# Optimization experiments

Hardware: AMD Instinct MI355X
Metric: run time of the kernel (lower is better)

## Reference

```python
import jax, jax.numpy as jnp
import numpy as np

N_NODES = 100000
DEG = 16
D_IN = 128
D_OUT = 128


def setup_inputs() -> dict:
    key = jax.random.key(0)
    k1, k2, k3, k4, k5, k6 = jax.random.split(key, 6)
    neighbours = jax.random.randint(k1, (N_NODES, DEG), 0, N_NODES, dtype=jnp.int64 if jax.config.jax_enable_x64 else jnp.int32)
    shape_features = jax.random.normal(k2, (N_NODES, D_IN), dtype=jnp.float32)
    scale = 1.0 / np.sqrt(D_IN)
    W1 = jax.random.normal(k3, (D_OUT, D_IN), dtype=jnp.float32) * scale
    b1 = jax.random.normal(k4, (D_OUT,), dtype=jnp.float32) * scale
    W2 = jax.random.normal(k5, (D_OUT, D_IN), dtype=jnp.float32) * scale
    b2 = jax.random.normal(k6, (D_OUT,), dtype=jnp.float32) * scale
    return {"neighbours": neighbours, "shape_features": shape_features,
            "W1": W1, "b1": b1, "W2": W2, "b2": b2}


def reference(neighbours, shape_features, W1, b1, W2, b2):
    # linear1(x): x @ W1^T + b1  -> [N, D_OUT]
    out1 = jnp.einsum('nd,od->no', shape_features, W1) + b1
    # per-node neighbor gather + sum (vectorized form of the Python loop)
    # gathered: [N, DEG, D_IN], aggr: [N, D_IN]
    aggr = shape_features[neighbours].sum(axis=1)
    out = out1 + jnp.einsum('nd,od->no', aggr, W2) + b2
    return jax.nn.relu(out)
```

## Files before the change

kernel.cpp:

```cpp
#include <hip/hip_runtime.h>
#include <hip/hip_bf16.h>
#include <stdint.h>


#define N_NODES 100000
#define DEG 16
#define KTOT 256
#define M_PAD 100096

typedef __attribute__((ext_vector_type(8))) short short8;
typedef __attribute__((ext_vector_type(4))) float floatx4;

static __device__ __forceinline__ unsigned short f2bf(float f) {
  union { float f; uint32_t u; } v; v.f = f;
  uint32_t u = v.u;
  return (unsigned short)((u + 0x7fffu + ((u >> 16) & 1u)) >> 16);
}
static __device__ __forceinline__ float bf2f(uint32_t bits16) {
  union { uint32_t u; float f; } v; v.u = bits16 << 16; return v.f;
}

__global__ __launch_bounds__(256) void k_prep(const float* __restrict__ W1, const float* __restrict__ b1,
                                              const float* __restrict__ W2, const float* __restrict__ b2,
                                              unsigned short* __restrict__ Bt, float* __restrict__ bias) {
  int t = blockIdx.x * 256 + threadIdx.x;
  int o = t >> 8, k = t & 255;
  float v = (k < 128) ? W1[o * 128 + k] : W2[o * 128 + (k - 128)];
  Bt[t] = f2bf(v);
  if (t < 128) bias[t] = b1[t] + b2[t];
}

__global__ __launch_bounds__(256) void k_convert(const float* __restrict__ x,
                                                 unsigned short* __restrict__ A) {
  int t = blockIdx.x * 256 + threadIdx.x;
  if (t >= N_NODES * 32) return;
  int n = t >> 5, c4 = t & 31;
  float4 v = *(const float4*)(x + (size_t)n * 128 + (size_t)c4 * 4);
  ushort4 o;
  o.x = f2bf(v.x); o.y = f2bf(v.y); o.z = f2bf(v.z); o.w = f2bf(v.w);
  *(ushort4*)(A + (size_t)n * 256 + (size_t)c4 * 4) = o;
}

__global__ __launch_bounds__(256) void k_aggr(const int* __restrict__ nbrs,
                                              unsigned short* __restrict__ A) {
  int gid = blockIdx.x * 4 + (threadIdx.x >> 6);
  int lane = threadIdx.x & 63;
  int myidx = nbrs[(size_t)gid * DEG + (lane & 15)];
  float a0 = 0.f, a1 = 0.f;
#pragma unroll
  for (int j = 0; j < DEG; ++j) {
    int nb = __shfl(myidx, j);
    uint32_t pv = *(const uint32_t*)(A + (size_t)nb * 256 + (size_t)lane * 2);
    a0 += bf2f(pv & 0xffffu);
    a1 += bf2f(pv >> 16);
  }
  uint32_t w = (uint32_t)f2bf(a0) | ((uint32_t)f2bf(a1) << 16);
  *(uint32_t*)(A + (size_t)gid * 256 + 128 + (size_t)lane * 2) = w;
}

__global__ __launch_bounds__(256) void k_gemm(const unsigned short* __restrict__ A,
                                              const unsigned short* __restrict__ Bt,
                                              const float* __restrict__ bias,
                                              float* __restrict__ out) {
  __shared__ unsigned short lds[16384];
  const int tid = threadIdx.x;
  const int lane = tid & 63;
  const int w = tid >> 6;
  const int wm = w >> 1, wn = w & 1;
  const size_t tile_m = (size_t)blockIdx.x * 128;

  floatx4 acc[4][4];
#pragma unroll
  for (int i = 0; i < 4; ++i)
#pragma unroll
    for (int j = 0; j < 4; ++j) acc[i][j] = (floatx4){0.f, 0.f, 0.f, 0.f};

  const int l8 = lane >> 3;
  const int slot_sw = (lane & 7) ^ l8;
  const unsigned short* Ag = A + tile_m * 256;

  for (int kt = 0; kt < 4; ++kt) {
    __syncthreads();
#pragma unroll
    for (int p = 0; p < 4; ++p) {
      int row = p * 32 + w * 8 + l8;
      const unsigned short* g = Ag + (size_t)row * 256 + kt * 64 + slot_sw * 8;
      __builtin_amdgcn_global_load_lds((const __attribute__((address_space(1))) uint32_t*)g,
                                       (__attribute__((address_space(3))) uint32_t*)&lds[(p * 4 + w) * 512],
                                       16, 0, 0);
    }
#pragma unroll
    for (int p = 0; p < 4; ++p) {
      int row = p * 32 + w * 8 + l8;
      const unsigned short* g = Bt + (size_t)row * 256 + kt * 64 + slot_sw * 8;
      __builtin_amdgcn_global_load_lds((const __attribute__((address_space(1))) uint32_t*)g,
                                       (__attribute__((address_space(3))) uint32_t*)&lds[8192 + (p * 4 + w) * 512],
                                       16, 0, 0);
    }
    __syncthreads();

#pragma unroll
    for (int ks = 0; ks < 2; ++ks) {
      short8 a[4], b[4];
      const int kb = ks * 64 + (lane >> 4) * 16;
      const int swz = (lane & 7) << 4;
#pragma unroll
      for (int mi = 0; mi < 4; ++mi) {
        int row = wm * 64 + mi * 16 + (lane & 15);
        a[mi] = *(const short8*)((const char*)lds + row * 128 + (kb ^ swz));
      }
#pragma unroll
      for (int ni = 0; ni < 4; ++ni) {
        int row = wn * 64 + ni * 16 + (lane & 15);
        b[ni] = *(const short8*)((const char*)lds + 16384 + row * 128 + (kb ^ swz));
      }
#pragma unroll
      for (int mi = 0; mi < 4; ++mi)
#pragma unroll
        for (int ni = 0; ni < 4; ++ni)
          acc[mi][ni] = __builtin_amdgcn_mfma_f32_16x16x32_bf16(a[mi], b[ni], acc[mi][ni], 0, 0, 0);
    }
  }

  float bcol[4];
#pragma unroll
  for (int ni = 0; ni < 4; ++ni) bcol[ni] = bias[wn * 64 + ni * 16 + (lane & 15)];
  const int r0 = (lane >> 4) * 4;
#pragma unroll
  for (int mi = 0; mi < 4; ++mi) {
    size_t mbase = tile_m + wm * 64 + mi * 16 + r0;
#pragma unroll
    for (int r = 0; r < 4; ++r) {
      size_t mrow = mbase + r;
      if (mrow < N_NODES) {
        float* orow = out + mrow * 128 + wn * 64 + (lane & 15);
#pragma unroll
        for (int ni = 0; ni < 4; ++ni) {
          float vv = acc[mi][ni][r] + bcol[ni];
          orow[ni * 16] = vv > 0.f ? vv : 0.f;
        }
      }
    }
  }
}

extern "C" void kernel_launch(void* const* d_in, const int* in_sizes, int n_in,
                              void* d_out, int out_size, void* d_ws, size_t ws_size,
                              hipStream_t stream) {
  const int* nbrs  = (const int*)d_in[0];
  const float* x   = (const float*)d_in[1];
  const float* W1  = (const float*)d_in[2];
  const float* b1  = (const float*)d_in[3];
  const float* W2  = (const float*)d_in[4];
  const float* b2  = (const float*)d_in[5];
  float* out = (float*)d_out;

  unsigned short* A  = (unsigned short*)d_ws;
  unsigned short* Bt = A + (size_t)M_PAD * 256;
  float* bias = (float*)(Bt + 128 * 256);

  k_prep<<<128, 256, 0, stream>>>(W1, b1, W2, b2, Bt, bias);
  k_convert<<<12500, 256, 0, stream>>>(x, A);
  k_aggr<<<25000, 256, 0, stream>>>(nbrs, A);
  k_gemm<<<782, 256, 0, stream>>>(A, Bt, bias, out);
}
```

Baseline: 183.2 us.

## Fuse neighbour aggregation into GEMM tile and merge weight prep into convert

The neighbour gather-sum now runs inside the GEMM kernel. Each block aggregates its 128 nodes straight into LDS as bf16 and feeds them to MFMA as the second half of K, so the separate aggregation kernel and its global write and re-read of the aggregated half of A go away. The bf16 feature buffer shrinks to 128 columns, weight and bias prep is folded into the convert kernel as extra blocks, and B fragments are loaded straight from global memory instead of being staged through LDS. MFMA runs at raised wave priority, with occupancy set to 3 blocks per CU. The cost is that the GEMM can no longer start until each block has done its own latency-bound gathers, and it now uses 48KB of LDS per block.

```diff
diff --git a/kernel.cpp b/kernel.cpp
--- a/kernel.cpp
+++ b/kernel.cpp
@@ -1,11 +1,9 @@
 #include <hip/hip_runtime.h>
-#include <hip/hip_bf16.h>
 #include <stdint.h>
 
 
 #define N_NODES 100000
 #define DEG 16
-#define KTOT 256
 #define M_PAD 100096
 
 typedef __attribute__((ext_vector_type(8))) short short8;
@@ -20,54 +18,96 @@
   union { uint32_t u; float f; } v; v.u = bits16 << 16; return v.f;
 }
 
-__global__ __launch_bounds__(256) void k_prep(const float* __restrict__ W1, const float* __restrict__ b1,
-                                              const float* __restrict__ W2, const float* __restrict__ b2,
-                                              unsigned short* __restrict__ Bt, float* __restrict__ bias) {
-  int t = blockIdx.x * 256 + threadIdx.x;
-  int o = t >> 8, k = t & 255;
-  float v = (k < 128) ? W1[o * 128 + k] : W2[o * 128 + (k - 128)];
-  Bt[t] = f2bf(v);
-  if (t < 128) bias[t] = b1[t] + b2[t];
+__global__ __launch_bounds__(256) void k_convert(const float* __restrict__ x,
+                                                 unsigned short* __restrict__ Xb,
+                                                 const float* __restrict__ W1, const float* __restrict__ b1,
+                                                 const float* __restrict__ W2, const float* __restrict__ b2,
+                                                 unsigned short* __restrict__ Bt, float* __restrict__ bias) {
+  int b = blockIdx.x;
+  if (b < 12500) {
+    int t = b * 256 + threadIdx.x;
+    int n = t >> 5, c4 = t & 31;
+    float4 v = *(const float4*)(x + (size_t)n * 128 + (size_t)c4 * 4);
+    ushort4 o;
+    o.x = f2bf(v.x); o.y = f2bf(v.y); o.z = f2bf(v.z); o.w = f2bf(v.w);
+    *(ushort4*)(Xb + (size_t)n * 128 + (size_t)c4 * 4) = o;
+  } else {
+    int t = (b - 12500) * 256 + threadIdx.x;
+    int o = t >> 8, k = t & 255;
+    float v = (k < 128) ? W1[o * 128 + k] : W2[o * 128 + (k - 128)];
+    Bt[t] = f2bf(v);
+    if (t < 128) bias[t] = b1[t] + b2[t];
+  }
 }
 
-__global__ __launch_bounds__(256) void k_convert(const float* __restrict__ x,
-                                                 unsigned short* __restrict__ A) {
-  int t = blockIdx.x * 256 + threadIdx.x;
-  if (t >= N_NODES * 32) return;
-  int n = t >> 5, c4 = t & 31;
-  float4 v = *(const float4*)(x + (size_t)n * 128 + (size_t)c4 * 4);
-  ushort4 o;
-  o.x = f2bf(v.x); o.y = f2bf(v.y); o.z = f2bf(v.z); o.w = f2bf(v.w);
-  *(ushort4*)(A + (size_t)n * 256 + (size_t)c4 * 4) = o;
-}
-
-__global__ __launch_bounds__(256) void k_aggr(const int* __restrict__ nbrs,
-                                              unsigned short* __restrict__ A) {
-  int gid = blockIdx.x * 4 + (threadIdx.x >> 6);
-  int lane = threadIdx.x & 63;
-  int myidx = nbrs[(size_t)gid * DEG + (lane & 15)];
-  float a0 = 0.f, a1 = 0.f;
-#pragma unroll
-  for (int j = 0; j < DEG; ++j) {
-    int nb = __shfl(myidx, j);
-    uint32_t pv = *(const uint32_t*)(A + (size_t)nb * 256 + (size_t)lane * 2);
-    a0 += bf2f(pv & 0xffffu);
-    a1 += bf2f(pv >> 16);
-  }
-  uint32_t w = (uint32_t)f2bf(a0) | ((uint32_t)f2bf(a1) << 16);
-  *(uint32_t*)(A + (size_t)gid * 256 + 128 + (size_t)lane * 2) = w;
-}
-
-__global__ __launch_bounds__(256) void k_gemm(const unsigned short* __restrict__ A,
-                                              const unsigned short* __restrict__ Bt,
-                                              const float* __restrict__ bias,
-                                              float* __restrict__ out) {
-  __shared__ unsigned short lds[16384];
+__global__ __launch_bounds__(256, 3) void k_fused(const int* __restrict__ nbrs,
+                                                  const unsigned short* __restrict__ Xb,
+                                                  const unsigned short* __restrict__ Bt,
+                                                  const float* __restrict__ bias,
+                                                  float* __restrict__ out) {
+  __shared__ uint4 smem4[3072];
+  char* aggr = (char*)smem4;
+  char* xbuf = (char*)smem4 + 32768;
   const int tid = threadIdx.x;
   const int lane = tid & 63;
   const int w = tid >> 6;
   const int wm = w >> 1, wn = w & 1;
-  const size_t tile_m = (size_t)blockIdx.x * 128;
+  const int q16 = lane >> 4, c16 = lane & 15;
+  const size_t tile = (size_t)blockIdx.x * 128;
+  const char* Xbb = (const char*)Xb;
+  const char* Btb = (const char*)Bt;
+
+  float bcol[4];
+#pragma unroll
+  for (int ni = 0; ni < 4; ++ni) bcol[ni] = bias[wn * 64 + ni * 16 + (lane & 15)];
+
+  auto STAGE = [&](int kt) {
+    int g = ((lane & 7) ^ (lane >> 3)) * 16;
+#pragma unroll
+    for (int s = 0; s < 4; ++s) {
+      int br = w * 32 + s * 8;
+      const char* src = Xbb + (tile + br + (lane >> 3)) * 256 + kt * 128 + g;
+      __builtin_amdgcn_global_load_lds((const __attribute__((address_space(1))) uint32_t*)src,
+                                       (__attribute__((address_space(3))) uint32_t*)(xbuf + br * 128),
+                                       16, 0, 0);
+    }
+  };
+
+  STAGE(0);
+
+  for (int r = 0; r < 8; ++r) {
+    int nodeb = (int)tile + w * 32 + r * 4;
+    int gi = nodeb * 16 + lane;
+    int midx = (gi < N_NODES * DEG) ? nbrs[gi] : 0;
+#pragma unroll
+    for (int q = 0; q < 4; ++q) {
+      int row = w * 32 + r * 4 + q;
+      float a8[8] = {0.f, 0.f, 0.f, 0.f, 0.f, 0.f, 0.f, 0.f};
+#pragma unroll
+      for (int i = 0; i < 4; ++i) {
+        int nb = __shfl(midx, q * 16 + i * 4 + q16);
+        uint4 pv = *(const uint4*)(Xbb + (size_t)nb * 256 + c16 * 16);
+        a8[0] += bf2f(pv.x & 0xffffu); a8[1] += bf2f(pv.x >> 16);
+        a8[2] += bf2f(pv.y & 0xffffu); a8[3] += bf2f(pv.y >> 16);
+        a8[4] += bf2f(pv.z & 0xffffu); a8[5] += bf2f(pv.z >> 16);
+        a8[6] += bf2f(pv.w & 0xffffu); a8[7] += bf2f(pv.w >> 16);
+      }
+#pragma unroll
+      for (int k = 0; k < 8; ++k) {
+        a8[k] += __shfl_xor(a8[k], 16);
+        a8[k] += __shfl_xor(a8[k], 32);
+      }
+      if (lane < 16) {
+        bool valid = (tile + row) < N_NODES;
+        uint4 wv;
+        wv.x = valid ? ((uint32_t)f2bf(a8[0]) | ((uint32_t)f2bf(a8[1]) << 16)) : 0u;
+        wv.y = valid ? ((uint32_t)f2bf(a8[2]) | ((uint32_t)f2bf(a8[3]) << 16)) : 0u;
+        wv.z = valid ? ((uint32_t)f2bf(a8[4]) | ((uint32_t)f2bf(a8[5]) << 16)) : 0u;
+        wv.w = valid ? ((uint32_t)f2bf(a8[6]) | ((uint32_t)f2bf(a8[7]) << 16)) : 0u;
+        *(uint4*)(aggr + row * 256 + ((c16 ^ (row & 7)) * 16)) = wv;
+      }
+    }
+  }
 
   floatx4 acc[4][4];
 #pragma unroll
@@ -75,60 +115,50 @@
 #pragma unroll
     for (int j = 0; j < 4; ++j) acc[i][j] = (floatx4){0.f, 0.f, 0.f, 0.f};
 
-  const int l8 = lane >> 3;
-  const int slot_sw = (lane & 7) ^ l8;
-  const unsigned short* Ag = A + tile_m * 256;
-
-  for (int kt = 0; kt < 4; ++kt) {
-    __syncthreads();
-#pragma unroll
-    for (int p = 0; p < 4; ++p) {
-      int row = p * 32 + w * 8 + l8;
-      const unsigned short* g = Ag + (size_t)row * 256 + kt * 64 + slot_sw * 8;
-      __builtin_amdgcn_global_load_lds((const __attribute__((address_space(1))) uint32_t*)g,
-                                       (__attribute__((address_space(3))) uint32_t*)&lds[(p * 4 + w) * 512],
-                                       16, 0, 0);
-    }
-#pragma unroll
-    for (int p = 0; p < 4; ++p) {
-      int row = p * 32 + w * 8 + l8;
-      const unsigned short* g = Bt + (size_t)row * 256 + kt * 64 + slot_sw * 8;
-      __builtin_amdgcn_global_load_lds((const __attribute__((address_space(1))) uint32_t*)g,
-                                       (__attribute__((address_space(3))) uint32_t*)&lds[8192 + (p * 4 + w) * 512],
-                                       16, 0, 0);
-    }
-    __syncthreads();
-
+  auto COMP = [&](int kt, int from_aggr) {
 #pragma unroll
     for (int ks = 0; ks < 2; ++ks) {
       short8 a[4], b[4];
-      const int kb = ks * 64 + (lane >> 4) * 16;
-      const int swz = (lane & 7) << 4;
 #pragma unroll
       for (int mi = 0; mi < 4; ++mi) {
         int row = wm * 64 + mi * 16 + (lane & 15);
-        a[mi] = *(const short8*)((const char*)lds + row * 128 + (kb ^ swz));
+        if (from_aggr) {
+          int slot = (kt - 2) * 8 + ks * 4 + q16;
+          a[mi] = *(const short8*)(aggr + row * 256 + ((slot ^ (lane & 7)) * 16));
+        } else {
+          int k8 = ks * 4 + q16;
+          a[mi] = *(const short8*)(xbuf + row * 128 + ((k8 ^ (lane & 7)) * 16));
+        }
       }
 #pragma unroll
       for (int ni = 0; ni < 4; ++ni) {
-        int row = wn * 64 + ni * 16 + (lane & 15);
-        b[ni] = *(const short8*)((const char*)lds + 16384 + row * 128 + (kb ^ swz));
+        int o = wn * 64 + ni * 16 + (lane & 15);
+        int slot = kt * 8 + ks * 4 + q16;
+        b[ni] = *(const short8*)(Btb + (size_t)o * 512 + slot * 16);
       }
+      __builtin_amdgcn_s_setprio(1);
 #pragma unroll
       for (int mi = 0; mi < 4; ++mi)
 #pragma unroll
         for (int ni = 0; ni < 4; ++ni)
           acc[mi][ni] = __builtin_amdgcn_mfma_f32_16x16x32_bf16(a[mi], b[ni], acc[mi][ni], 0, 0, 0);
+      __builtin_amdgcn_s_setprio(0);
     }
-  }
+  };
 
-  float bcol[4];
-#pragma unroll
-  for (int ni = 0; ni < 4; ++ni) bcol[ni] = bias[wn * 64 + ni * 16 + (lane & 15)];
+  __syncthreads();
+  COMP(0, 0);
+  __syncthreads();
+  STAGE(1);
+  COMP(2, 1);
+  __syncthreads();
+  COMP(1, 0);
+  COMP(3, 1);
+
   const int r0 = (lane >> 4) * 4;
 #pragma unroll
   for (int mi = 0; mi < 4; ++mi) {
-    size_t mbase = tile_m + wm * 64 + mi * 16 + r0;
+    size_t mbase = tile + wm * 64 + mi * 16 + r0;
 #pragma unroll
     for (int r = 0; r < 4; ++r) {
       size_t mrow = mbase + r;
@@ -155,12 +185,10 @@
   const float* b2  = (const float*)d_in[5];
   float* out = (float*)d_out;
 
-  unsigned short* A  = (unsigned short*)d_ws;
-  unsigned short* Bt = A + (size_t)M_PAD * 256;
+  unsigned short* Xb = (unsigned short*)d_ws;
+  unsigned short* Bt = Xb + (size_t)M_PAD * 128;
   float* bias = (float*)(Bt + 128 * 256);
 
-  k_prep<<<128, 256, 0, stream>>>(W1, b1, W2, b2, Bt, bias);
-  k_convert<<<12500, 256, 0, stream>>>(x, A);
-  k_aggr<<<25000, 256, 0, stream>>>(nbrs, A);
-  k_gemm<<<782, 256, 0, stream>>>(A, Bt, bias, out);
+  k_convert<<<12628, 256, 0, stream>>>(x, Xb, W1, b1, W2, b2, Bt, bias);
+  k_fused<<<782, 256, 0, stream>>>(nbrs, Xb, Bt, bias, out);
 }
```

New measurement: 207.4 us. 1.13x slower.
